# Kernel tuning notes

Measured on AMD Instinct MI355X. Metric: run time of the kernel, lower is better.

The kernel has to match this reference:

```python
import jax, jax.numpy as jnp
import numpy as np

N_NODES = 50000
N_EDGES = 800000
N_LABEL_EDGES = 200000
IN_CH = 256
HID = 64
OUT_CH = 64


def gcn_conv(x, W, b, edge_index, n_nodes):
    """PyG GCNConv: symmetric-normalized aggregation with self-loops.
    out[col] = sum_row norm(row,col) * (x @ W)[row] + b
    """
    xw = x @ W  # [N, out]
    loops = jnp.arange(n_nodes, dtype=edge_index.dtype)
    row = jnp.concatenate([edge_index[0], loops])  # source
    col = jnp.concatenate([edge_index[1], loops])  # target
    deg = jax.ops.segment_sum(jnp.ones_like(col, dtype=xw.dtype), col, num_segments=n_nodes)
    dis = jnp.where(deg > 0, jax.lax.rsqrt(deg), 0.0)
    norm = dis[row] * dis[col]  # [E+N]
    out = jax.ops.segment_sum(xw[row] * norm[:, None], col, num_segments=n_nodes)
    return out + b


def setup_inputs() -> dict:
    key = jax.random.key(0)
    k0, k1, k2, k3, k4 = jax.random.split(key, 5)
    x = jax.random.normal(k0, (N_NODES, IN_CH), dtype=jnp.float32)
    edge_index = jax.random.randint(k1, (2, N_EDGES), 0, N_NODES, dtype=jnp.int32)
    edge_label_index = jax.random.randint(k2, (2, N_LABEL_EDGES), 0, N_NODES, dtype=jnp.int32)
    W1 = jax.random.normal(k3, (IN_CH, HID), dtype=jnp.float32) * (1.0 / np.sqrt(IN_CH))
    b1 = jnp.zeros((HID,), dtype=jnp.float32)
    W2 = jax.random.normal(k4, (HID, OUT_CH), dtype=jnp.float32) * (1.0 / np.sqrt(HID))
    b2 = jnp.zeros((OUT_CH,), dtype=jnp.float32)
    return {"x": x, "edge_index": edge_index, "edge_label_index": edge_label_index,
            "W1": W1, "b1": b1, "W2": W2, "b2": b2}


def reference(x, edge_index, edge_label_index, W1, b1, W2, b2):
    n = x.shape[0]
    # encode: two GCNConv layers with ReLU between
    h = jax.nn.relu(gcn_conv(x, W1, b1, edge_index, n))
    z = gcn_conv(h, W2, b2, edge_index, n)
    # decode: gather node pairs, elementwise multiply, sum over features
    src, dst = edge_label_index[0], edge_label_index[1]
    return jnp.sum(z[src] * z[dst], axis=1)  # [N_LABEL_EDGES]
```

## Files before the change

### kernel.cpp

```cpp
#include <hip/hip_runtime.h>
#include <hip/hip_bf16.h>


constexpr int NC = 256;
constexpr int NBPAD = 256;
constexpr int BSHIFT = 8;

__device__ __forceinline__ unsigned short f2bf(float f) {
    unsigned u = __float_as_uint(f);
    return (unsigned short)((u + 0x7FFF + ((u >> 16) & 1)) >> 16);
}
__device__ __forceinline__ float bf2f(unsigned short h) {
    return __uint_as_float(((unsigned)h) << 16);
}
__device__ __forceinline__ float4 bf4_to_f4(ushort4 u) {
    return make_float4(bf2f(u.x), bf2f(u.y), bf2f(u.z), bf2f(u.w));
}

__global__ __launch_bounds__(256) void hist_kernel(const int* __restrict__ col,
                                                   int* __restrict__ hist, int E, int CE) {
    __shared__ int hl[NBPAD];
    const int t = threadIdx.x, c = blockIdx.x;
    hl[t] = 0;
    __syncthreads();
    const int s = c * CE, e = min(E, s + CE);
    for (int i = s + t; i < e; i += 256) atomicAdd(&hl[col[i] >> BSHIFT], 1);
    __syncthreads();
    hist[t * NC + c] = hl[t];
}

__global__ __launch_bounds__(256) void bsum_kernel(const int* __restrict__ hist,
                                                   int* __restrict__ bsums) {
    __shared__ int red[256];
    const int t = threadIdx.x, b = blockIdx.x;
    red[t] = hist[b * NC + t];
    __syncthreads();
    for (int off = 128; off > 0; off >>= 1) {
        if (t < off) red[t] += red[t + off];
        __syncthreads();
    }
    if (t == 0) bsums[b] = red[0];
}

__global__ __launch_bounds__(256) void bscan_kernel(int* __restrict__ bsums) {
    __shared__ int sc[256];
    const int t = threadIdx.x;
    const int v = bsums[t];
    sc[t] = v;
    __syncthreads();
    for (int off = 1; off < 256; off <<= 1) {
        int u = (t >= off) ? sc[t - off] : 0;
        __syncthreads();
        sc[t] += u;
        __syncthreads();
    }
    bsums[t] = sc[t] - v;
}

__global__ __launch_bounds__(256) void rowscan_kernel(int* __restrict__ hist,
                                                      const int* __restrict__ bsums) {
    __shared__ int sc[256];
    const int t = threadIdx.x, b = blockIdx.x;
    const int v = hist[b * NC + t];
    sc[t] = v;
    __syncthreads();
    for (int off = 1; off < 256; off <<= 1) {
        int u = (t >= off) ? sc[t - off] : 0;
        __syncthreads();
        sc[t] += u;
        __syncthreads();
    }
    hist[b * NC + t] = sc[t] - v + bsums[b];
}

__global__ __launch_bounds__(256) void reorder_kernel(const int* __restrict__ row,
                                                      const int* __restrict__ col,
                                                      const int* __restrict__ hist,
                                                      int2* __restrict__ part, int E, int CE) {
    __shared__ int cur[NBPAD];
    const int t = threadIdx.x, c = blockIdx.x;
    cur[t] = hist[t * NC + c];
    __syncthreads();
    const int s = c * CE, e = min(E, s + CE);
    for (int i = s + t; i < e; i += 256) {
        const int r = row[i], cl = col[i];
        const int p = atomicAdd(&cur[cl >> BSHIFT], 1);
        part[p] = make_int2(r, cl);
    }
}

__global__ __launch_bounds__(256) void bucket_csr_kernel(const int2* __restrict__ part,
                                                         const int* __restrict__ hist,
                                                         int* __restrict__ csr,
                                                         int* __restrict__ offs,
                                                         float* __restrict__ dis,
                                                         int N, int E, int nbk) {
    __shared__ int cnt[256];
    __shared__ int sc[256];
    const int t = threadIdx.x, b = blockIdx.x;
    const int base = b << BSHIFT;
    const int bstart = hist[b * NC];
    const int bend = (b + 1 < NBPAD) ? hist[(b + 1) * NC] : E;
    const int m = bend - bstart;
    cnt[t] = 0;
    __syncthreads();
    for (int i = t; i < m; i += 256) atomicAdd(&cnt[part[bstart + i].y - base], 1);
    __syncthreads();
    const int v = cnt[t];
    sc[t] = v;
    __syncthreads();
    for (int off = 1; off < 256; off <<= 1) {
        int u = (t >= off) ? sc[t - off] : 0;
        __syncthreads();
        sc[t] += u;
        __syncthreads();
    }
    const int excl = sc[t] - v;
    const int node = base + t;
    if (node < N) {
        offs[node] = bstart + excl;
        dis[node] = rsqrtf((float)(v + 1));
    }
    sc[t] = excl;
    __syncthreads();
    for (int i = t; i < m; i += 256) {
        const int2 ec = part[bstart + i];
        const int p = atomicAdd(&sc[ec.y - base], 1);
        csr[bstart + p] = ec.x;
    }
    if (b == nbk - 1 && t == 0) offs[N] = E;
}

template <int K>
__global__ __launch_bounds__(256) void gemm_tile(const float* __restrict__ X,
                                                 const float* __restrict__ W,
                                                 const float* __restrict__ rowscale,
                                                 unsigned short* __restrict__ Y, int nrows) {
    __shared__ float sX[64 * 64];
    __shared__ float sW[64 * 64];
    const int tid = threadIdx.x;
    const int tx = tid & 15;
    const int ty = tid >> 4;
    const int rowbase = blockIdx.x * 64;

    float acc[16];
    #pragma unroll
    for (int i = 0; i < 16; ++i) acc[i] = 0.f;

    const int lr = tid & 63;
    const int lq = tid >> 6;
    int grow = rowbase + lr;
    if (grow >= nrows) grow = nrows - 1;
    const float* xrow = X + (long)grow * K;

    for (int kc = 0; kc < K; kc += 64) {
        if (kc) __syncthreads();
        #pragma unroll
        for (int i = 0; i < 4; ++i) {
            const int o = tid * 4 + i * 1024;
            *(float4*)&sW[o] = *(const float4*)&W[(long)kc * 64 + o];
        }
        #pragma unroll
        for (int t = 0; t < 4; ++t) {
            const int k = lq * 16 + t * 4;
            const float4 v = *(const float4*)&xrow[kc + k];
            sX[(k + 0) * 64 + lr] = v.x;
            sX[(k + 1) * 64 + lr] = v.y;
            sX[(k + 2) * 64 + lr] = v.z;
            sX[(k + 3) * 64 + lr] = v.w;
        }
        __syncthreads();
        #pragma unroll 4
        for (int k = 0; k < 64; ++k) {
            const float4 xv = *(const float4*)&sX[k * 64 + ty * 4];
            const float4 wv = *(const float4*)&sW[k * 64 + tx * 4];
            acc[0]  = fmaf(xv.x, wv.x, acc[0]);
            acc[1]  = fmaf(xv.x, wv.y, acc[1]);
            acc[2]  = fmaf(xv.x, wv.z, acc[2]);
            acc[3]  = fmaf(xv.x, wv.w, acc[3]);
            acc[4]  = fmaf(xv.y, wv.x, acc[4]);
            acc[5]  = fmaf(xv.y, wv.y, acc[5]);
            acc[6]  = fmaf(xv.y, wv.z, acc[6]);
            acc[7]  = fmaf(xv.y, wv.w, acc[7]);
            acc[8]  = fmaf(xv.z, wv.x, acc[8]);
            acc[9]  = fmaf(xv.z, wv.y, acc[9]);
            acc[10] = fmaf(xv.z, wv.z, acc[10]);
            acc[11] = fmaf(xv.z, wv.w, acc[11]);
            acc[12] = fmaf(xv.w, wv.x, acc[12]);
            acc[13] = fmaf(xv.w, wv.y, acc[13]);
            acc[14] = fmaf(xv.w, wv.z, acc[14]);
            acc[15] = fmaf(xv.w, wv.w, acc[15]);
        }
    }

    #pragma unroll
    for (int i = 0; i < 4; ++i) {
        const int orow = rowbase + ty * 4 + i;
        if (orow < nrows) {
            const float d = rowscale[orow];
            ushort4 ov;
            ov.x = f2bf(d * acc[i * 4 + 0]);
            ov.y = f2bf(d * acc[i * 4 + 1]);
            ov.z = f2bf(d * acc[i * 4 + 2]);
            ov.w = f2bf(d * acc[i * 4 + 3]);
            *(ushort4*)&Y[(long)orow * 64 + tx * 4] = ov;
        }
    }
}

template <bool RELU, bool OUT_BF16>
__global__ __launch_bounds__(256) void agg_kernel(const unsigned short* __restrict__ xs,
                                                  const int* __restrict__ csr,
                                                  const int* __restrict__ offs,
                                                  const float* __restrict__ dis,
                                                  const float* __restrict__ bias,
                                                  void* __restrict__ out, int n) {
    __shared__ int sidx[4][64];
    const int wv = threadIdx.x >> 6;
    const int lane = threadIdx.x & 63;
    const int grp = lane >> 4;
    const int fl = lane & 15;
    const int i = blockIdx.x * 4 + wv;
    if (i >= n) return;
    float4 acc = make_float4(0.f, 0.f, 0.f, 0.f);
    if (grp == 0)
        acc = bf4_to_f4(*(const ushort4*)&xs[(long)i * 64 + fl * 4]);
    const int s = offs[i];
    const int e = offs[i + 1];
    for (int jb = s; jb < e; jb += 64) {
        const int nb = min(64, e - jb);
        if (lane < nb) sidx[wv][lane] = csr[jb + lane];
        int u = grp;
        for (; u + 4 < nb; u += 8) {
            const int r0 = sidx[wv][u];
            const int r1 = sidx[wv][u + 4];
            const float4 v0 = bf4_to_f4(*(const ushort4*)&xs[(long)r0 * 64 + fl * 4]);
            const float4 v1 = bf4_to_f4(*(const ushort4*)&xs[(long)r1 * 64 + fl * 4]);
            acc.x += v0.x + v1.x; acc.y += v0.y + v1.y;
            acc.z += v0.z + v1.z; acc.w += v0.w + v1.w;
        }
        for (; u < nb; u += 4) {
            const int r0 = sidx[wv][u];
            const float4 v0 = bf4_to_f4(*(const ushort4*)&xs[(long)r0 * 64 + fl * 4]);
            acc.x += v0.x; acc.y += v0.y; acc.z += v0.z; acc.w += v0.w;
        }
    }
    acc.x += __shfl_xor(acc.x, 16); acc.y += __shfl_xor(acc.y, 16);
    acc.z += __shfl_xor(acc.z, 16); acc.w += __shfl_xor(acc.w, 16);
    acc.x += __shfl_xor(acc.x, 32); acc.y += __shfl_xor(acc.y, 32);
    acc.z += __shfl_xor(acc.z, 32); acc.w += __shfl_xor(acc.w, 32);
    if (grp == 0) {
        const float di = dis[i];
        const float4 b = *(const float4*)&bias[fl * 4];
        float4 o;
        o.x = fmaf(acc.x, di, b.x); o.y = fmaf(acc.y, di, b.y);
        o.z = fmaf(acc.z, di, b.z); o.w = fmaf(acc.w, di, b.w);
        if (RELU) {
            o.x = fmaxf(o.x, 0.f); o.y = fmaxf(o.y, 0.f);
            o.z = fmaxf(o.z, 0.f); o.w = fmaxf(o.w, 0.f);
        }
        if (OUT_BF16) {
            ushort4 ov;
            ov.x = f2bf(o.x); ov.y = f2bf(o.y); ov.z = f2bf(o.z); ov.w = f2bf(o.w);
            *(ushort4*)&((unsigned short*)out)[(long)i * 64 + fl * 4] = ov;
        } else {
            *(float4*)&((float*)out)[(long)i * 64 + fl * 4] = o;
        }
    }
}

__global__ __launch_bounds__(256) void decode_kernel(const unsigned short* __restrict__ z,
                                                     const int* __restrict__ src,
                                                     const int* __restrict__ dst,
                                                     float* __restrict__ out, int L) {
    const int t = blockIdx.x * 256 + threadIdx.x;
    const int e = t >> 4;
    const int fl = t & 15;
    if (e >= L) return;
    const int s = src[e];
    const int d = dst[e];
    const float4 a = bf4_to_f4(*(const ushort4*)&z[(long)s * 64 + fl * 4]);
    const float4 b = bf4_to_f4(*(const ushort4*)&z[(long)d * 64 + fl * 4]);
    float p = a.x * b.x + a.y * b.y + a.z * b.z + a.w * b.w;
    p += __shfl_xor(p, 8); p += __shfl_xor(p, 4);
    p += __shfl_xor(p, 2); p += __shfl_xor(p, 1);
    if (fl == 0) out[e] = p;
}

extern "C" void kernel_launch(void* const* d_in, const int* in_sizes, int n_in,
                              void* d_out, int out_size, void* d_ws, size_t ws_size,
                              hipStream_t stream) {
    const float* x   = (const float*)d_in[0];
    const int*   ei  = (const int*)d_in[1];
    const int*   eli = (const int*)d_in[2];
    const float* W1  = (const float*)d_in[3];
    const float* b1  = (const float*)d_in[4];
    const float* W2  = (const float*)d_in[5];
    const float* b2  = (const float*)d_in[6];
    float* out = (float*)d_out;

    const int N = in_sizes[0] / 256;
    const int E = in_sizes[1] / 2;
    const int L = in_sizes[2] / 2;
    const int* row = ei;
    const int* col = ei + E;
    const int* src = eli;
    const int* dst = eli + L;

    char* w = (char*)d_ws;
    unsigned short* xs = (unsigned short*)w;  w += (size_t)N * 64 * 2;
    float* h   = (float*)w;  w += (size_t)N * 64 * 4;
    unsigned short* z = (unsigned short*)w;  w += (size_t)N * 64 * 2;
    int*   csr = (int*)w;    w += (size_t)E * 4;
    int*   offs = (int*)w;   w += (size_t)(N + 1) * 4;
    float* dis = (float*)w;  w += (size_t)N * 4;
    int2*  part = (int2*)w;  w += (size_t)E * 8;
    int*  hist  = (int*)h;
    int*  bsums = hist + NBPAD * NC;

    const int CE = (E + NC - 1) / NC;
    const int nbk = (N + (1 << BSHIFT) - 1) >> BSHIFT;

    hist_kernel<<<NC, 256, 0, stream>>>(col, hist, E, CE);
    bsum_kernel<<<NBPAD, 256, 0, stream>>>(hist, bsums);
    bscan_kernel<<<1, 256, 0, stream>>>(bsums);
    rowscan_kernel<<<NBPAD, 256, 0, stream>>>(hist, bsums);
    reorder_kernel<<<NC, 256, 0, stream>>>(row, col, hist, part, E, CE);
    bucket_csr_kernel<<<nbk, 256, 0, stream>>>(part, hist, csr, offs, dis, N, E, nbk);

    gemm_tile<256><<<(N + 63) / 64, 256, 0, stream>>>(x, W1, dis, xs, N);
    agg_kernel<true, false><<<(N + 3) / 4, 256, 0, stream>>>(xs, csr, offs, dis, b1, h, N);
    gemm_tile<64><<<(N + 63) / 64, 256, 0, stream>>>(h, W2, dis, xs, N);
    agg_kernel<false, true><<<(N + 3) / 4, 256, 0, stream>>>(xs, csr, offs, dis, b2, z, N);
    decode_kernel<<<(L + 15) / 16, 256, 0, stream>>>(z, src, dst, out, L);
}
```

Before: 223.2 us.

## Fuse bucket-sum into histogram and merge scan kernels for edge partitioning

The histogram kernel now accumulates per-bucket totals with global atomics, which removes the separate bucket-sum and single-block scan kernels. Each rowscan block computes its own base by reducing the preceding bucket totals, and the number of chunks doubles to 512, with each thread scanning two chunk counts. The aim is fewer kernel launches and dependent steps in the CSR build, plus more parallelism in the histogram and reorder passes. The cost is a memset, global atomics, extra workspace, and redundant prefix reductions in every rowscan block.

```diff
diff --git a/kernel.cpp b/kernel.cpp
--- a/kernel.cpp
+++ b/kernel.cpp
@@ -2,7 +2,7 @@
 #include <hip/hip_bf16.h>
 
 
-constexpr int NC = 256;
+constexpr int NC = 512;
 constexpr int NBPAD = 256;
 constexpr int BSHIFT = 8;
 
@@ -18,7 +18,8 @@
 }
 
 __global__ __launch_bounds__(256) void hist_kernel(const int* __restrict__ col,
-                                                   int* __restrict__ hist, int E, int CE) {
+                                                   int* __restrict__ histCM,
+                                                   int* __restrict__ bsums, int E, int CE) {
     __shared__ int hl[NBPAD];
     const int t = threadIdx.x, c = blockIdx.x;
     hl[t] = 0;
@@ -26,27 +27,28 @@
     const int s = c * CE, e = min(E, s + CE);
     for (int i = s + t; i < e; i += 256) atomicAdd(&hl[col[i] >> BSHIFT], 1);
     __syncthreads();
-    hist[t * NC + c] = hl[t];
-}
-
-__global__ __launch_bounds__(256) void bsum_kernel(const int* __restrict__ hist,
-                                                   int* __restrict__ bsums) {
+    const int v = hl[t];
+    histCM[c * NBPAD + t] = v;
+    if (v) atomicAdd(&bsums[t], v);
+}
+
+__global__ __launch_bounds__(256) void rowscan_kernel(const int* __restrict__ histCM,
+                                                      const int* __restrict__ bsums,
+                                                      int* __restrict__ offsBM) {
     __shared__ int red[256];
+    __shared__ int sc[256];
     const int t = threadIdx.x, b = blockIdx.x;
-    red[t] = hist[b * NC + t];
+    red[t] = (t < b) ? bsums[t] : 0;
     __syncthreads();
     for (int off = 128; off > 0; off >>= 1) {
         if (t < off) red[t] += red[t + off];
         __syncthreads();
     }
-    if (t == 0) bsums[b] = red[0];
-}
-
-__global__ __launch_bounds__(256) void bscan_kernel(int* __restrict__ bsums) {
-    __shared__ int sc[256];
-    const int t = threadIdx.x;
-    const int v = bsums[t];
-    sc[t] = v;
+    const int base = red[0];
+    const int a0 = histCM[(2 * t) * NBPAD + b];
+    const int a1 = histCM[(2 * t + 1) * NBPAD + b];
+    const int ps = a0 + a1;
+    sc[t] = ps;
     __syncthreads();
     for (int off = 1; off < 256; off <<= 1) {
         int u = (t >= off) ? sc[t - off] : 0;
@@ -54,32 +56,18 @@
         sc[t] += u;
         __syncthreads();
     }
-    bsums[t] = sc[t] - v;
-}
-
-__global__ __launch_bounds__(256) void rowscan_kernel(int* __restrict__ hist,
-                                                      const int* __restrict__ bsums) {
-    __shared__ int sc[256];
-    const int t = threadIdx.x, b = blockIdx.x;
-    const int v = hist[b * NC + t];
-    sc[t] = v;
-    __syncthreads();
-    for (int off = 1; off < 256; off <<= 1) {
-        int u = (t >= off) ? sc[t - off] : 0;
-        __syncthreads();
-        sc[t] += u;
-        __syncthreads();
-    }
-    hist[b * NC + t] = sc[t] - v + bsums[b];
+    const int excl = sc[t] - ps;
+    offsBM[b * NC + 2 * t] = base + excl;
+    offsBM[b * NC + 2 * t + 1] = base + excl + a0;
 }
 
 __global__ __launch_bounds__(256) void reorder_kernel(const int* __restrict__ row,
                                                       const int* __restrict__ col,
-                                                      const int* __restrict__ hist,
+                                                      const int* __restrict__ offsBM,
                                                       int2* __restrict__ part, int E, int CE) {
     __shared__ int cur[NBPAD];
     const int t = threadIdx.x, c = blockIdx.x;
-    cur[t] = hist[t * NC + c];
+    cur[t] = offsBM[t * NC + c];
     __syncthreads();
     const int s = c * CE, e = min(E, s + CE);
     for (int i = s + t; i < e; i += 256) {
@@ -90,7 +78,7 @@
 }
 
 __global__ __launch_bounds__(256) void bucket_csr_kernel(const int2* __restrict__ part,
-                                                         const int* __restrict__ hist,
+                                                         const int* __restrict__ offsBM,
                                                          int* __restrict__ csr,
                                                          int* __restrict__ offs,
                                                          float* __restrict__ dis,
@@ -99,8 +87,8 @@
     __shared__ int sc[256];
     const int t = threadIdx.x, b = blockIdx.x;
     const int base = b << BSHIFT;
-    const int bstart = hist[b * NC];
-    const int bend = (b + 1 < NBPAD) ? hist[(b + 1) * NC] : E;
+    const int bstart = offsBM[b * NC];
+    const int bend = (b + 1 < NBPAD) ? offsBM[(b + 1) * NC] : E;
     const int m = bend - bstart;
     cnt[t] = 0;
     __syncthreads();
@@ -315,18 +303,18 @@
     int*   offs = (int*)w;   w += (size_t)(N + 1) * 4;
     float* dis = (float*)w;  w += (size_t)N * 4;
     int2*  part = (int2*)w;  w += (size_t)E * 8;
-    int*  hist  = (int*)h;
-    int*  bsums = hist + NBPAD * NC;
+    int* histCM = (int*)w;   w += (size_t)NC * NBPAD * 4;
+    int* offsBM = (int*)w;   w += (size_t)NBPAD * NC * 4;
+    int* bsums  = (int*)w;   w += NBPAD * 4;
 
     const int CE = (E + NC - 1) / NC;
     const int nbk = (N + (1 << BSHIFT) - 1) >> BSHIFT;
 
-    hist_kernel<<<NC, 256, 0, stream>>>(col, hist, E, CE);
-    bsum_kernel<<<NBPAD, 256, 0, stream>>>(hist, bsums);
-    bscan_kernel<<<1, 256, 0, stream>>>(bsums);
-    rowscan_kernel<<<NBPAD, 256, 0, stream>>>(hist, bsums);
-    reorder_kernel<<<NC, 256, 0, stream>>>(row, col, hist, part, E, CE);
-    bucket_csr_kernel<<<nbk, 256, 0, stream>>>(part, hist, csr, offs, dis, N, E, nbk);
+    hipMemsetAsync(bsums, 0, NBPAD * sizeof(int), stream);
+    hist_kernel<<<NC, 256, 0, stream>>>(col, histCM, bsums, E, CE);
+    rowscan_kernel<<<NBPAD, 256, 0, stream>>>(histCM, bsums, offsBM);
+    reorder_kernel<<<NC, 256, 0, stream>>>(row, col, offsBM, part, E, CE);
+    bucket_csr_kernel<<<nbk, 256, 0, stream>>>(part, offsBM, csr, offs, dis, N, E, nbk);
 
     gemm_tile<256><<<(N + 63) / 64, 256, 0, stream>>>(x, W1, dis, xs, N);
     agg_kernel<true, false><<<(N + 3) / 4, 256, 0, stream>>>(xs, csr, offs, dis, b1, h, N);
```

Result: slower. 235.1 us (+5.3%).
